# Performance work log

Measured on AMD Instinct MI355X. Metric: run time of the kernel, lower is better.

The kernel has to match this reference:

```python
import jax, jax.numpy as jnp
import numpy as np
from math import factorial, sqrt, pi

MAX_DEG = 4
CUTOFF = 5.0

# ---------- Clebsch-Gordan coefficients for real spherical harmonics ----------

def _cg_complex(j1, m1, j2, m2, j3, m3):
    if m1 + m2 != m3 or j3 < abs(j1 - j2) or j3 > j1 + j2:
        return 0.0
    f = factorial
    pre = sqrt((2 * j3 + 1) * f(j1 + j2 - j3) * f(j1 - j2 + j3) * f(-j1 + j2 + j3) / f(j1 + j2 + j3 + 1))
    pre *= sqrt(f(j1 + m1) * f(j1 - m1) * f(j2 + m2) * f(j2 - m2) * f(j3 + m3) * f(j3 - m3))
    s = 0.0
    for k in range(0, j1 + j2 + j3 + 1):
        t = [k, j1 + j2 - j3 - k, j1 - m1 - k, j2 + m2 - k, j3 - j2 + m1 + k, j3 - j1 - m2 + k]
        if min(t) < 0:
            continue
        s += (-1) ** k / (f(t[0]) * f(t[1]) * f(t[2]) * f(t[3]) * f(t[4]) * f(t[5]))
    return pre * s


def _u_matrix(l):
    # complex->real spherical-harmonic change of basis, U[m_real+l, mu+l]
    U = np.zeros((2 * l + 1, 2 * l + 1), dtype=np.complex128)
    U[l, l] = 1.0
    inv_sqrt2 = 1.0 / sqrt(2.0)
    for m in range(1, l + 1):
        U[l + m, l + m] = ((-1) ** m) * inv_sqrt2
        U[l + m, l - m] = inv_sqrt2
        U[l - m, l - m] = 1j * inv_sqrt2
        U[l - m, l + m] = -1j * ((-1) ** m) * inv_sqrt2
    return U


def _real_cg(l1, l2, l3):
    C = np.zeros((2 * l1 + 1, 2 * l2 + 1, 2 * l3 + 1), dtype=np.complex128)
    for m1 in range(-l1, l1 + 1):
        for m2 in range(-l2, l2 + 1):
            m3 = m1 + m2
            if -l3 <= m3 <= l3:
                C[m1 + l1, m2 + l2, m3 + l3] = _cg_complex(l1, m1, l2, m2, l3, m3)
    R = np.einsum('ai,bj,ck,ijk->abc', _u_matrix(l1), _u_matrix(l2), _u_matrix(l3).conj(), C)
    return np.real(R).astype(np.float32)

# Parity-even coupling paths (l1+l2+l3 even), all degrees <= MAX_DEG -> 42 paths
CG_PATHS = []
for _l1 in range(MAX_DEG + 1):
    for _l2 in range(MAX_DEG + 1):
        for _l3 in range(abs(_l1 - _l2), min(MAX_DEG, _l1 + _l2) + 1):
            if (_l1 + _l2 + _l3) % 2 == 0:
                CG_PATHS.append((_l1, _l2, _l3, _real_cg(_l1, _l2, _l3)))
NUM_PATHS = len(CG_PATHS)  # 42


def _sl(l):
    return slice(l * l, (l + 1) * (l + 1))


def tensor_product(x1, x2, w):
    # x1, x2: (E, 1, 25, F); w: (NUM_PATHS, F). One learnable weight per path per channel.
    blocks = [None] * (MAX_DEG + 1)
    for p, (l1, l2, l3, cg) in enumerate(CG_PATHS):
        a = x1[..., _sl(l1), :]
        b = x2[..., _sl(l2), :]
        c = jnp.einsum('...if,...jf,ijk->...kf', a, b, jnp.asarray(cg)) * w[p]
        blocks[l3] = c if blocks[l3] is None else blocks[l3] + c
    return jnp.concatenate(blocks, axis=-2)


def real_sph(u):
    # u: (E,3) unit vectors -> (E, 25) real orthonormal spherical harmonics, index l*l+l+m
    x, y, z = u[..., 0], u[..., 1], u[..., 2]
    L = MAX_DEG
    Cm = [jnp.ones_like(x)]
    Sm = [jnp.zeros_like(x)]
    for m in range(1, L + 1):
        Cm.append(x * Cm[m - 1] - y * Sm[m - 1])
        Sm.append(x * Sm[m - 1] + y * Cm[m - 1])
    Q = {(0, 0): jnp.ones_like(z)}
    for m in range(L + 1):
        if m > 0:
            Q[(m, m)] = (2 * m - 1) * Q[(m - 1, m - 1)]
        if m + 1 <= L:
            Q[(m + 1, m)] = (2 * m + 1) * z * Q[(m, m)]
        for l in range(m + 2, L + 1):
            Q[(l, m)] = ((2 * l - 1) * z * Q[(l - 1, m)] - (l + m - 1) * Q[(l - 2, m)]) / (l - m)
    ys = []
    for l in range(L + 1):
        row = [None] * (2 * l + 1)
        row[l] = sqrt((2 * l + 1) / (4 * pi)) * Q[(l, 0)]
        for m in range(1, l + 1):
            Klm = sqrt((2 * l + 1) / (4 * pi) * factorial(l - m) / factorial(l + m))
            base = sqrt(2.0) * Klm * Q[(l, m)]
            row[l + m] = base * Cm[m]
            row[l - m] = base * Sm[m]
        ys.extend(row)
    return jnp.stack(ys, axis=-1)


def bond_basis(disp, cutoff, num):
    # sinc radial basis * cosine cutoff * spherical harmonics -> (E, 1, 25, num)
    r = jnp.sqrt(jnp.sum(disp * disp, axis=-1) + 1e-12)
    Y = real_sph(disp / r[..., None])  # (E, 25)
    k = jnp.arange(1, num + 1, dtype=disp.dtype)
    rad = jnp.sinc(r[..., None] * k / cutoff)  # (E, num)
    cut = jnp.where(r < cutoff, 0.5 * (1.0 + jnp.cos(np.float32(np.pi) * r / cutoff)), 0.0)
    out = Y[..., :, None] * rad[..., None, :] * cut[..., None, None]
    return out[:, None, :, :]


def setup_inputs() -> dict:
    key = jax.random.key(0)
    k1, k2, k3, k4, k5, k6 = jax.random.split(key, 6)
    N, E, F = 10000, 160000, 16
    return {
        'atomic_descriptors': jax.random.normal(k1, (N, 1, 25, F), dtype=jnp.float32),
        'neighbour_displacements': jax.random.normal(k2, (E, 3), dtype=jnp.float32),
        'weights1': jax.random.normal(k3, (NUM_PATHS, F), dtype=jnp.float32),
        'weights2': jax.random.normal(k4, (NUM_PATHS, F), dtype=jnp.float32),
        'neighbours_i': jax.random.randint(k5, (E,), 0, N, dtype=jnp.int32),
        'neighbours_j': jax.random.randint(k6, (E,), 0, N, dtype=jnp.int32),
    }


def reference(atomic_descriptors, neighbour_displacements, weights1, weights2, neighbours_i, neighbours_j):
    F = atomic_descriptors.shape[-1]
    a1 = atomic_descriptors[neighbours_i]  # (E,1,25,F) irregular gather
    a2 = atomic_descriptors[neighbours_j]
    y = tensor_product(a1, a2, weights1)  # first equivariant CG tensor product
    bexp = bond_basis(neighbour_displacements, CUTOFF, F)  # radial x angular bond basis
    return tensor_product(y, bexp, weights2)
```

## Files before the change

### kernel.cpp

```cpp
#include <hip/hip_runtime.h>

namespace cg {

constexpr double FACT[16] = {
  1.0, 1.0, 2.0, 6.0, 24.0, 120.0, 720.0, 5040.0, 40320.0, 362880.0,
  3628800.0, 39916800.0, 479001600.0, 6227020800.0, 87178291200.0,
  1307674368000.0 };

constexpr double csqrt_(double x){
  if (x <= 0.0) return 0.0;
  double xx = x, g = 1.0;
  while (xx >= 256.0)      { xx *= (1.0/256.0); g *= 16.0;       }
  while (xx >= 4.0)        { xx *= 0.25;        g *= 2.0;        }
  while (xx < (1.0/256.0)) { xx *= 256.0;       g *= (1.0/16.0); }
  while (xx < 1.0)         { xx *= 4.0;         g *= 0.5;        }
  double s = 1.5;
  for (int i = 0; i < 10; ++i) s = 0.5*(s + xx/s);
  return g*s;
}

constexpr double cg_complex(int j1,int m1,int j2,int m2,int j3,int m3){
  if (m1+m2 != m3) return 0.0;
  int dj = j1-j2; if (dj < 0) dj = -dj;
  if (j3 < dj || j3 > j1+j2) return 0.0;
  if (m1<-j1||m1>j1||m2<-j2||m2>j2||m3<-j3||m3>j3) return 0.0;
  double pre = csqrt_((2.0*j3+1.0)*FACT[j1+j2-j3]*FACT[j1-j2+j3]*FACT[-j1+j2+j3]/FACT[j1+j2+j3+1]);
  pre *= csqrt_(FACT[j1+m1]*FACT[j1-m1]*FACT[j2+m2]*FACT[j2-m2]*FACT[j3+m3]*FACT[j3-m3]);
  double s = 0.0;
  for (int k = 0; k <= j1+j2+j3; ++k){
    int t1=j1+j2-j3-k, t2=j1-m1-k, t3=j2+m2-k, t4=j3-j2+m1+k, t5=j3-j1-m2+k;
    if (t1<0||t2<0||t3<0||t4<0||t5<0) continue;
    double term = 1.0/(FACT[k]*FACT[t1]*FACT[t2]*FACT[t3]*FACT[t4]*FACT[t5]);
    s += (k & 1) ? -term : term;
  }
  return pre*s;
}

struct URow { int n; int col[2]; double re[2]; double im[2]; };

constexpr URow urow(int l, int a){
  URow r{};
  const double is2 = 0.70710678118654752440;
  int m = a - l;
  if (m == 0){
    r.n = 1; r.col[0] = l; r.re[0] = 1.0; r.im[0] = 0.0;
  } else if (m > 0){
    r.n = 2;
    r.col[0] = l+m; r.re[0] = (m & 1) ? -is2 : is2; r.im[0] = 0.0;
    r.col[1] = l-m; r.re[1] = is2;                  r.im[1] = 0.0;
  } else {
    int mm = -m; r.n = 2;
    r.col[0] = l-mm; r.re[0] = 0.0; r.im[0] = is2;
    r.col[1] = l+mm; r.re[1] = 0.0; r.im[1] = (mm & 1) ? is2 : -is2;
  }
  return r;
}

struct PTab {
  int nnz;
  unsigned char ia[192];
  unsigned char jb[192];
  unsigned char kc[192];
  float v[192];
};

constexpr PTab build_path(int l1, int l2, int l3){
  double Cc[9][9] = {};
  for (int i = 0; i < 2*l1+1; ++i)
    for (int j = 0; j < 2*l2+1; ++j){
      int m3 = (i-l1)+(j-l2);
      Cc[i][j] = (m3 >= -l3 && m3 <= l3)
               ? cg_complex(l1, i-l1, l2, j-l2, l3, m3) : 0.0;
    }
  PTab t{};
  for (int a = 0; a < 2*l1+1; ++a)
    for (int b = 0; b < 2*l2+1; ++b)
      for (int c = 0; c < 2*l3+1; ++c){
        URow ra = urow(l1,a), rb = urow(l2,b), rc = urow(l3,c);
        double re = 0.0;
        for (int x = 0; x < ra.n; ++x)
          for (int yy = 0; yy < rb.n; ++yy){
            double pr = ra.re[x]*rb.re[yy] - ra.im[x]*rb.im[yy];
            double pi = ra.re[x]*rb.im[yy] + ra.im[x]*rb.re[yy];
            for (int z = 0; z < rc.n; ++z){
              if (rc.col[z]-l3 != (ra.col[x]-l1)+(rb.col[yy]-l2)) continue;
              double ure = pr*rc.re[z] + pi*rc.im[z];
              re += ure * Cc[ra.col[x]][rb.col[yy]];
            }
          }
        if (re > 1e-10 || re < -1e-10){
          t.ia[t.nnz] = (unsigned char)a;
          t.jb[t.nnz] = (unsigned char)b;
          t.kc[t.nnz] = (unsigned char)c;
          t.v[t.nnz]  = (float)re;
          t.nnz++;
        }
      }
  return t;
}

constexpr double PI_D = 3.14159265358979323846264338327950288;
constexpr double Kd(int l, int m){
  double v = csqrt_((2.0*l+1.0)/(4.0*PI_D)*FACT[l-m]/FACT[l+m]);
  if (m) v *= csqrt_(2.0);
  return v;
}

}

#define PATHS_X(X) \
  X(0,0,0,0) X(1,0,1,1) X(2,0,2,2) X(3,0,3,3) X(4,0,4,4) \
  X(5,1,0,1) X(6,1,1,0) X(7,1,1,2) X(8,1,2,1) X(9,1,2,3) X(10,1,3,2) X(11,1,3,4) X(12,1,4,3) \
  X(13,2,0,2) X(14,2,1,1) X(15,2,1,3) X(16,2,2,0) X(17,2,2,2) X(18,2,2,4) X(19,2,3,1) X(20,2,3,3) X(21,2,4,2) X(22,2,4,4) \
  X(23,3,0,3) X(24,3,1,2) X(25,3,1,4) X(26,3,2,1) X(27,3,2,3) X(28,3,3,0) X(29,3,3,2) X(30,3,3,4) X(31,3,4,1) X(32,3,4,3) \
  X(33,4,0,4) X(34,4,1,3) X(35,4,2,2) X(36,4,2,4) X(37,4,3,1) X(38,4,3,3) X(39,4,4,0) X(40,4,4,2) X(41,4,4,4)

#define DECL_TAB(P,L1,L2,L3) static constexpr cg::PTab CGT_##P = cg::build_path(L1,L2,L3);
PATHS_X(DECL_TAB)
#undef DECL_TAB

static constexpr float K00=(float)cg::Kd(0,0);
static constexpr float K10=(float)cg::Kd(1,0), K11=(float)cg::Kd(1,1);
static constexpr float K20=(float)cg::Kd(2,0), K21=(float)cg::Kd(2,1), K22=(float)cg::Kd(2,2);
static constexpr float K30=(float)cg::Kd(3,0), K31=(float)cg::Kd(3,1), K32=(float)cg::Kd(3,2), K33=(float)cg::Kd(3,3);
static constexpr float K40=(float)cg::Kd(4,0), K41=(float)cg::Kd(4,1), K42=(float)cg::Kd(4,2), K43=(float)cg::Kd(4,3), K44=(float)cg::Kd(4,4);

static constexpr float PI_F = 3.14159274101257324f;

__global__ __launch_bounds__(256, 4) void bctmd_kernel(
    const float* __restrict__ A,
    const float* __restrict__ D,
    const float* __restrict__ W1,
    const float* __restrict__ W2,
    const int*   __restrict__ NI,
    const int*   __restrict__ NJ,
    float* __restrict__ out,
    int E)
{
  int g = blockIdx.x * 256 + threadIdx.x;
  int e = g >> 4;
  int f = g & 15;
  if (e >= E) return;

  const float* __restrict__ a1p = A + (size_t)NI[e] * 400 + f;
  const float* __restrict__ a2p = A + (size_t)NJ[e] * 400 + f;

  float a1[25], a2[25];
#pragma unroll
  for (int i = 0; i < 25; ++i) a1[i] = a1p[i*16];
#pragma unroll
  for (int i = 0; i < 25; ++i) a2[i] = a2p[i*16];

  float y[25];
#pragma unroll
  for (int i = 0; i < 25; ++i) y[i] = 0.f;

#define TP1(P,L1,L2,L3) { \
    float part[2*(L3)+1]; \
    _Pragma("unroll") for (int k = 0; k < 2*(L3)+1; ++k) part[k] = 0.f; \
    _Pragma("unroll") \
    for (int t = 0; t < CGT_##P.nnz; ++t) \
      part[CGT_##P.kc[t]] += CGT_##P.v[t] * a1[(L1)*(L1)+CGT_##P.ia[t]] * a2[(L2)*(L2)+CGT_##P.jb[t]]; \
    const float wp = W1[(P)*16 + f]; \
    _Pragma("unroll") for (int k = 0; k < 2*(L3)+1; ++k) y[(L3)*(L3)+k] += wp * part[k]; \
  }
  PATHS_X(TP1)
#undef TP1

  float dx = D[3*e], dy = D[3*e+1], dz = D[3*e+2];
  float r2 = dx*dx + dy*dy + dz*dz + 1e-12f;
  float inv = __builtin_amdgcn_rsqf(r2);
  float r   = r2 * inv;
  float ux = dx*inv, uy = dy*inv, uz = dz*inv;

  float Ys[25];
  {
    float C1 = ux,            S1 = uy;
    float C2 = ux*C1 - uy*S1, S2 = ux*S1 + uy*C1;
    float C3 = ux*C2 - uy*S2, S3 = ux*S2 + uy*C2;
    float C4 = ux*C3 - uy*S3, S4 = ux*S3 + uy*C3;
    float z = uz;
    float Q00 = 1.f;
    float Q11 = 1.f, Q22 = 3.f, Q33 = 15.f, Q44 = 105.f;
    float Q10 = z, Q21 = 3.f*z, Q32 = 15.f*z, Q43 = 105.f*z;
    float Q20 = 0.5f*(3.f*z*Q10 - Q00);
    float Q31 = 0.5f*(5.f*z*Q21 - 3.f*Q11);
    float Q42 = 0.5f*(7.f*z*Q32 - 5.f*Q22);
    float Q30 = (5.f*z*Q20 - 2.f*Q10)*(1.f/3.f);
    float Q41 = (7.f*z*Q31 - 4.f*Q21)*(1.f/3.f);
    float Q40 = 0.25f*(7.f*z*Q30 - 3.f*Q20);

    Ys[0]  = K00*Q00;
    Ys[1]  = K11*Q11*S1;  Ys[2]  = K10*Q10;     Ys[3]  = K11*Q11*C1;
    Ys[4]  = K22*Q22*S2;  Ys[5]  = K21*Q21*S1;  Ys[6]  = K20*Q20;
    Ys[7]  = K21*Q21*C1;  Ys[8]  = K22*Q22*C2;
    Ys[9]  = K33*Q33*S3;  Ys[10] = K32*Q32*S2;  Ys[11] = K31*Q31*S1;
    Ys[12] = K30*Q30;     Ys[13] = K31*Q31*C1;  Ys[14] = K32*Q32*C2;
    Ys[15] = K33*Q33*C3;
    Ys[16] = K44*Q44*S4;  Ys[17] = K43*Q43*S3;  Ys[18] = K42*Q42*S2;
    Ys[19] = K41*Q41*S1;  Ys[20] = K40*Q40;     Ys[21] = K41*Q41*C1;
    Ys[22] = K42*Q42*C2;  Ys[23] = K43*Q43*C3;  Ys[24] = K44*Q44*C4;
  }

  float tt  = PI_F * r * (float)(f+1) * 0.2f;
  float rad = __sinf(tt) * __builtin_amdgcn_rcpf(tt);
  float cut = (r < 5.0f) ? 0.5f*(1.0f + __cosf(PI_F * r * 0.2f)) : 0.0f;
  float s   = rad * cut;

  float o[25];
#pragma unroll
  for (int i = 0; i < 25; ++i) o[i] = 0.f;

#define TP2(P,L1,L2,L3) { \
    float part[2*(L3)+1]; \
    _Pragma("unroll") for (int k = 0; k < 2*(L3)+1; ++k) part[k] = 0.f; \
    _Pragma("unroll") \
    for (int t = 0; t < CGT_##P.nnz; ++t) \
      part[CGT_##P.kc[t]] += CGT_##P.v[t] * y[(L1)*(L1)+CGT_##P.ia[t]] * Ys[(L2)*(L2)+CGT_##P.jb[t]]; \
    const float wp = W2[(P)*16 + f] * s; \
    _Pragma("unroll") for (int k = 0; k < 2*(L3)+1; ++k) o[(L3)*(L3)+k] += wp * part[k]; \
  }
  PATHS_X(TP2)
#undef TP2

  float* __restrict__ op = out + (size_t)e * 400 + f;
#pragma unroll
  for (int k = 0; k < 25; ++k) op[k*16] = o[k];
}

extern "C" void kernel_launch(void* const* d_in, const int* in_sizes, int n_in,
                              void* d_out, int out_size, void* d_ws, size_t ws_size,
                              hipStream_t stream) {
  const float* A  = (const float*)d_in[0];
  const float* D  = (const float*)d_in[1];
  const float* W1 = (const float*)d_in[2];
  const float* W2 = (const float*)d_in[3];
  const int*   NI = (const int*)d_in[4];
  const int*   NJ = (const int*)d_in[5];
  float* out = (float*)d_out;

  int E = in_sizes[4];
  long total = (long)E * 16;
  int block = 256;
  int grid = (int)((total + block - 1) / block);
  bctmd_kernel<<<grid, block, 0, stream>>>(A, D, W1, W2, NI, NJ, out, E);
}
```

Before: 235.8 us.

## Process two channels per thread with packed math and merged CG path groups

```diff
diff --git a/kernel.cpp b/kernel.cpp
--- a/kernel.cpp
+++ b/kernel.cpp
@@ -1,4 +1,6 @@
 #include <hip/hip_runtime.h>
+
+typedef float v2f __attribute__((ext_vector_type(2)));
 
 namespace cg {
 
@@ -119,6 +121,85 @@
 PATHS_X(DECL_TAB)
 #undef DECL_TAB
 
+struct GTab {
+  int n;
+  int ptot;
+  unsigned int zmask;
+  unsigned char i8[512], j8[512], kk[512];
+  bool np[512], ft[512];
+  float v[512];
+};
+
+constexpr GTab merge_group(int npaths,
+                           const cg::PTab* t0, int l30,
+                           const cg::PTab* t1, int l31,
+                           const cg::PTab* t2, int l32){
+  GTab g{};
+  const cg::PTab* ts[3] = {t0, t1, t2};
+  int ls[3] = {l30, l31, l32};
+  int pofs[3] = {0,0,0};
+  int acc = 0;
+  for (int s = 0; s < npaths; ++s){ pofs[s] = acc; acc += 2*ls[s]+1; }
+  g.ptot = acc;
+  bool touched[32] = {};
+  for (int j = 0; j < 9; ++j)
+    for (int i = 0; i < 9; ++i){
+      bool first = true;
+      for (int s = 0; s < npaths; ++s){
+        const cg::PTab* T = ts[s];
+        for (int t = 0; t < T->nnz; ++t){
+          if ((int)T->ia[t] == i && (int)T->jb[t] == j){
+            int kx = pofs[s] + (int)T->kc[t];
+            g.i8[g.n] = (unsigned char)i;
+            g.j8[g.n] = (unsigned char)j;
+            g.kk[g.n] = (unsigned char)kx;
+            g.np[g.n] = first; first = false;
+            g.ft[g.n] = !touched[kx]; touched[kx] = true;
+            g.v[g.n]  = T->v[t];
+            g.n++;
+          }
+        }
+      }
+    }
+  unsigned int zm = 0;
+  for (int k = 0; k < g.ptot; ++k) if (!touched[k]) zm |= (1u << k);
+  g.zmask = zm;
+  return g;
+}
+
+#define GROUPS_X(X) \
+  X(0,0, 1,  0,0,   0,0,   0,0) \
+  X(0,1, 1,  1,1,   1,1,   1,1) \
+  X(0,2, 1,  2,2,   2,2,   2,2) \
+  X(0,3, 1,  3,3,   3,3,   3,3) \
+  X(0,4, 1,  4,4,   4,4,   4,4) \
+  X(1,0, 1,  5,1,   5,1,   5,1) \
+  X(1,1, 2,  6,0,   7,2,   7,2) \
+  X(1,2, 2,  8,1,   9,3,   9,3) \
+  X(1,3, 2, 10,2,  11,4,  11,4) \
+  X(1,4, 1, 12,3,  12,3,  12,3) \
+  X(2,0, 1, 13,2,  13,2,  13,2) \
+  X(2,1, 2, 14,1,  15,3,  15,3) \
+  X(2,2, 3, 16,0,  17,2,  18,4) \
+  X(2,3, 2, 19,1,  20,3,  20,3) \
+  X(2,4, 2, 21,2,  22,4,  22,4) \
+  X(3,0, 1, 23,3,  23,3,  23,3) \
+  X(3,1, 2, 24,2,  25,4,  25,4) \
+  X(3,2, 2, 26,1,  27,3,  27,3) \
+  X(3,3, 3, 28,0,  29,2,  30,4) \
+  X(3,4, 2, 31,1,  32,3,  32,3) \
+  X(4,0, 1, 33,4,  33,4,  33,4) \
+  X(4,1, 1, 34,3,  34,3,  34,3) \
+  X(4,2, 2, 35,2,  36,4,  36,4) \
+  X(4,3, 2, 37,1,  38,3,  38,3) \
+  X(4,4, 3, 39,0,  40,2,  41,4)
+
+#define DECL_GROUP(L1,L2,NP,P0,L30,P1,L31,P2,L32) \
+  static constexpr GTab G_##L1##_##L2 = \
+    merge_group(NP, &CGT_##P0, L30, &CGT_##P1, L31, &CGT_##P2, L32);
+GROUPS_X(DECL_GROUP)
+#undef DECL_GROUP
+
 static constexpr float K00=(float)cg::Kd(0,0);
 static constexpr float K10=(float)cg::Kd(1,0), K11=(float)cg::Kd(1,1);
 static constexpr float K20=(float)cg::Kd(2,0), K21=(float)cg::Kd(2,1), K22=(float)cg::Kd(2,2);
@@ -127,7 +208,39 @@
 
 static constexpr float PI_F = 3.14159274101257324f;
 
-__global__ __launch_bounds__(256, 4) void bctmd_kernel(
+#define RUN_GROUP(GN,L1,L2,NP,P0,L30,P1,L31,P2,L32,S1,S2,DST,WEX) { \
+    v2f part[GN.ptot]; \
+    _Pragma("unroll") \
+    for (int k = 0; k < GN.ptot; ++k) if ((GN.zmask >> k) & 1u) part[k] = vzero; \
+    v2f prod = vzero; \
+    _Pragma("unroll") \
+    for (int t = 0; t < GN.n; ++t) { \
+      if (GN.np[t]) prod = S1[(L1)*(L1)+(int)GN.i8[t]] * S2[(L2)*(L2)+(int)GN.j8[t]]; \
+      if (GN.ft[t]) part[GN.kk[t]]  = GN.v[t] * prod; \
+      else          part[GN.kk[t]] += GN.v[t] * prod; \
+    } \
+    { const v2f wp = WEX(P0); \
+      _Pragma("unroll") for (int k = 0; k < 2*(L30)+1; ++k) \
+        DST[(L30)*(L30)+k] += wp * part[k]; } \
+    if constexpr ((NP) > 1) { const v2f wp = WEX(P1); \
+      _Pragma("unroll") for (int k = 0; k < 2*(L31)+1; ++k) \
+        DST[(L31)*(L31)+k] += wp * part[2*(L30)+1 + k]; } \
+    if constexpr ((NP) > 2) { const v2f wp = WEX(P2); \
+      _Pragma("unroll") for (int k = 0; k < 2*(L32)+1; ++k) \
+        DST[(L32)*(L32)+k] += wp * part[2*(L30)+1 + 2*(L31)+1 + k]; } \
+  }
+
+#define TP1W(P) (*(const v2f*)(W1p + (P)*16))
+#define TP2W(P) (sv * (*(const v2f*)(W2p + (P)*16)))
+
+#define TP1_G(L1,L2,NP,P0,L30,P1,L31,P2,L32) \
+  RUN_GROUP(G_##L1##_##L2, L1,L2,NP,P0,L30,P1,L31,P2,L32, a1,a2,y,TP1W)
+#define TP2_G(L1,L2,NP,P0,L30,P1,L31,P2,L32) \
+  RUN_GROUP(G_##L1##_##L2, L1,L2,NP,P0,L30,P1,L31,P2,L32, y,Ys,o,TP2W)
+
+__global__ __launch_bounds__(256)
+__attribute__((amdgpu_waves_per_eu(2, 2)))
+void bctmd_kernel(
     const float* __restrict__ A,
     const float* __restrict__ D,
     const float* __restrict__ W1,
@@ -137,35 +250,27 @@
     float* __restrict__ out,
     int E)
 {
-  int g = blockIdx.x * 256 + threadIdx.x;
-  int e = g >> 4;
-  int f = g & 15;
+  const v2f vzero = {0.f, 0.f};
+  int g  = blockIdx.x * 256 + threadIdx.x;
+  int e  = g >> 3;
+  int f2 = (g & 7) * 2;
   if (e >= E) return;
 
-  const float* __restrict__ a1p = A + (size_t)NI[e] * 400 + f;
-  const float* __restrict__ a2p = A + (size_t)NJ[e] * 400 + f;
-
-  float a1[25], a2[25];
-#pragma unroll
-  for (int i = 0; i < 25; ++i) a1[i] = a1p[i*16];
-#pragma unroll
-  for (int i = 0; i < 25; ++i) a2[i] = a2p[i*16];
-
-  float y[25];
-#pragma unroll
-  for (int i = 0; i < 25; ++i) y[i] = 0.f;
-
-#define TP1(P,L1,L2,L3) { \
-    float part[2*(L3)+1]; \
-    _Pragma("unroll") for (int k = 0; k < 2*(L3)+1; ++k) part[k] = 0.f; \
-    _Pragma("unroll") \
-    for (int t = 0; t < CGT_##P.nnz; ++t) \
-      part[CGT_##P.kc[t]] += CGT_##P.v[t] * a1[(L1)*(L1)+CGT_##P.ia[t]] * a2[(L2)*(L2)+CGT_##P.jb[t]]; \
-    const float wp = W1[(P)*16 + f]; \
-    _Pragma("unroll") for (int k = 0; k < 2*(L3)+1; ++k) y[(L3)*(L3)+k] += wp * part[k]; \
-  }
-  PATHS_X(TP1)
-#undef TP1
+  const float* __restrict__ a1p = A + (size_t)NI[e] * 400 + f2;
+  const float* __restrict__ a2p = A + (size_t)NJ[e] * 400 + f2;
+  const float* __restrict__ W1p = W1 + f2;
+  const float* __restrict__ W2p = W2 + f2;
+
+  v2f a1[25], a2[25];
+#pragma unroll
+  for (int i = 0; i < 25; ++i) a1[i] = *(const v2f*)(a1p + i*16);
+#pragma unroll
+  for (int i = 0; i < 25; ++i) a2[i] = *(const v2f*)(a2p + i*16);
+
+  v2f y[25];
+#pragma unroll
+  for (int i = 0; i < 25; ++i) y[i] = vzero;
+  GROUPS_X(TP1_G)
 
   float dx = D[3*e], dy = D[3*e+1], dz = D[3*e+2];
   float r2 = dx*dx + dy*dy + dz*dz + 1e-12f;
@@ -202,30 +307,22 @@
     Ys[22] = K42*Q42*C2;  Ys[23] = K43*Q43*C3;  Ys[24] = K44*Q44*C4;
   }
 
-  float tt  = PI_F * r * (float)(f+1) * 0.2f;
-  float rad = __sinf(tt) * __builtin_amdgcn_rcpf(tt);
-  float cut = (r < 5.0f) ? 0.5f*(1.0f + __cosf(PI_F * r * 0.2f)) : 0.0f;
-  float s   = rad * cut;
-
-  float o[25];
-#pragma unroll
-  for (int i = 0; i < 25; ++i) o[i] = 0.f;
-
-#define TP2(P,L1,L2,L3) { \
-    float part[2*(L3)+1]; \
-    _Pragma("unroll") for (int k = 0; k < 2*(L3)+1; ++k) part[k] = 0.f; \
-    _Pragma("unroll") \
-    for (int t = 0; t < CGT_##P.nnz; ++t) \
-      part[CGT_##P.kc[t]] += CGT_##P.v[t] * y[(L1)*(L1)+CGT_##P.ia[t]] * Ys[(L2)*(L2)+CGT_##P.jb[t]]; \
-    const float wp = W2[(P)*16 + f] * s; \
-    _Pragma("unroll") for (int k = 0; k < 2*(L3)+1; ++k) o[(L3)*(L3)+k] += wp * part[k]; \
-  }
-  PATHS_X(TP2)
-#undef TP2
-
-  float* __restrict__ op = out + (size_t)e * 400 + f;
-#pragma unroll
-  for (int k = 0; k < 25; ++k) op[k*16] = o[k];
+  float base = PI_F * r * 0.2f;
+  float tt0  = base * (float)(f2+1);
+  float tt1  = base * (float)(f2+2);
+  float rad0 = __sinf(tt0) * __builtin_amdgcn_rcpf(tt0);
+  float rad1 = __sinf(tt1) * __builtin_amdgcn_rcpf(tt1);
+  float cut  = (r < 5.0f) ? 0.5f*(1.0f + __cosf(base)) : 0.0f;
+  v2f sv; sv.x = rad0*cut; sv.y = rad1*cut;
+
+  v2f o[25];
+#pragma unroll
+  for (int i = 0; i < 25; ++i) o[i] = vzero;
+  GROUPS_X(TP2_G)
+
+  float* __restrict__ op = out + (size_t)e * 400 + f2;
+#pragma unroll
+  for (int k = 0; k < 25; ++k) *(v2f*)(op + k*16) = o[k];
 }
 
 extern "C" void kernel_launch(void* const* d_in, const int* in_sizes, int n_in,
@@ -240,7 +337,7 @@
   float* out = (float*)d_out;
 
   int E = in_sizes[4];
-  long total = (long)E * 16;
+  long total = (long)E * 8;
   int block = 256;
   int grid = (int)((total + block - 1) / block);
   bctmd_kernel<<<grid, block, 0, stream>>>(A, D, W1, W2, NI, NJ, out, E);
```

After: 285.5 us. +21.1%, slower.
